# Optimization experiments

Measured on AMD Instinct MI355X. Metric: run time of the kernel, lower is better.

## Reference

```python
import jax, jax.numpy as jnp
import numpy as np

B, T, C_EMB, C_HEAD = 4, 4096, 1024, 64

def setup_inputs() -> dict:
    key = jax.random.key(0)
    kx, kk, kq, kv = jax.random.split(key, 4)
    x = jax.random.normal(kx, (B, T, C_EMB), dtype=jnp.float32)
    # nn.Linear(C_EMB, C_HEAD, bias=False); store as (in, out) so projection is x @ W
    Wk = jax.random.normal(kk, (C_EMB, C_HEAD), dtype=jnp.float32) * 0.02
    Wq = jax.random.normal(kq, (C_EMB, C_HEAD), dtype=jnp.float32) * 0.02
    Wv = jax.random.normal(kv, (C_EMB, C_HEAD), dtype=jnp.float32) * 0.02
    return {"x": x, "Wk": Wk, "Wq": Wq, "Wv": Wv}

def reference(x, Wk, Wq, Wv):
    k = x @ Wk  # [B,T,Ch]
    q = x @ Wq
    v = x @ Wv
    scale = C_HEAD ** -0.5
    weights = jnp.einsum('bqc,bkc->bqk', q, k) * scale  # [B,T,T]
    causal = jnp.tril(jnp.ones((T, T), dtype=bool))
    weights = jnp.where(causal, weights, -jnp.inf)
    # NOTE: original uses F.softmax(dim=1), i.e. over the QUERY (row) axis -> axis=-2
    weights = jax.nn.softmax(weights, axis=-2)
    # dropout_rate=0.0 (eval) -> identity
    return jnp.einsum('bqk,bkc->bqc', weights, v)
```

## Files before the change

### kernel.cpp

```cpp
#include <hip/hip_runtime.h>
#include <math.h>

#define BB 4
#define TT 4096
#define CE 1024
#define CH 64
#define SCALE2 0.18033688011112042f
#define NQT 64
#define NZC 8
#define NZP 4

typedef unsigned short ushort_t;
typedef __attribute__((ext_vector_type(8))) short bf16x8;
typedef __attribute__((ext_vector_type(8))) unsigned short u16x8;
typedef __attribute__((ext_vector_type(4))) float f32x4;

__device__ __forceinline__ unsigned short f2bf(float f) {
    unsigned int x = __builtin_bit_cast(unsigned int, f);
    unsigned int r = x + 0x7fffu + ((x >> 16) & 1u);
    return (unsigned short)(r >> 16);
}
__device__ __forceinline__ float bf2f(unsigned short u) {
    unsigned int x = ((unsigned int)u) << 16;
    return __builtin_bit_cast(float, x);
}

__device__ __forceinline__ void stage_tile(const ushort_t* __restrict__ src,
                                           ushort_t (*dst)[68], int tg)
{
#pragma unroll
    for (int i = 0; i < 2; ++i) {
        const int idx = i * 256 + tg;
        const int row = idx >> 3, c0 = (idx & 7) * 8;
        u16x8 v = *(const u16x8*)(src + (long)idx * 8);
        union { u16x8 v; uint2 q[2]; } uu; uu.v = v;
        *(uint2*)&dst[row][c0]     = uu.q[0];
        *(uint2*)&dst[row][c0 + 4] = uu.q[1];
    }
}

__device__ __forceinline__ void stage_tile512(const ushort_t* __restrict__ src,
                                              ushort_t (*dst)[68], int tid)
{
    const int row = tid >> 3, c0 = (tid & 7) * 8;
    u16x8 v = *(const u16x8*)(src + (long)tid * 8);
    union { u16x8 v; uint2 q[2]; } uu; uu.v = v;
    *(uint2*)&dst[row][c0]     = uu.q[0];
    *(uint2*)&dst[row][c0 + 4] = uu.q[1];
}

__device__ __forceinline__ bf16x8 frag68(const ushort_t* p) {
    union { bf16x8 v; uint2 q[2]; } uu;
    uu.q[0] = *(const uint2*)p;
    uu.q[1] = *(const uint2*)(p + 4);
    return uu.v;
}

__global__ __launch_bounds__(256)
void wt_build(const float* __restrict__ Wk, const float* __restrict__ Wq,
              const float* __restrict__ Wv, ushort_t* __restrict__ wt2)
{
    const int m = blockIdx.x, kt = blockIdx.y;
    const float* __restrict__ W = (m == 0) ? Wk : (m == 1 ? Wq : Wv);
    const int k0 = kt * 64;
    __shared__ float lds[64][65];
    const int cc = threadIdx.x & 63, g = threadIdx.x >> 6;
#pragma unroll
    for (int i = 0; i < 16; ++i) {
        const int r = g * 16 + i;
        lds[r][cc] = W[(k0 + r) * CH + cc];
    }
    __syncthreads();
    const int k = k0 + cc;
#pragma unroll
    for (int i = 0; i < 16; ++i) {
        const int c = g * 16 + i;
        wt2[((long)(k >> 5) * 192 + (m * 64 + c)) * 32 + (k & 31)] = f2bf(lds[cc][c]);
    }
}

__global__ __launch_bounds__(512)
void proj_mfma(const float* __restrict__ x, const ushort_t* __restrict__ wt2,
               ushort_t* __restrict__ qb, ushort_t* __restrict__ kb, ushort_t* __restrict__ vb)
{
    const int tid = threadIdx.x;
    const int w = tid >> 6, l = tid & 63, lg = l >> 4, lr = l & 15;
    const int wr = w >> 2, wc = w & 3;
    const long t0 = (long)blockIdx.x * 32;

    __shared__ ushort_t As[32][68];
    __shared__ ushort_t Bs[192][68];

    f32x4 acc[3];
#pragma unroll
    for (int nf = 0; nf < 3; ++nf) acc[nf] = (f32x4){0.f, 0.f, 0.f, 0.f};

    const int arow = tid >> 4, acol = (tid & 15) * 4;
    const float* __restrict__ xsrc = x + (t0 + arow) * CE + acol;

    int bc[3], bh[3], bk[3];
#pragma unroll
    for (int i = 0; i < 3; ++i) {
        const int idx = i * 512 + tid;
        const int h = idx >= 768;
        const int j = idx - h * 768;
        bc[i] = j >> 2; bh[i] = h; bk[i] = (j & 3) * 8;
    }

    float4 a4 = *(const float4*)(xsrc);
    u16x8 bv[3];
#pragma unroll
    for (int i = 0; i < 3; ++i)
        bv[i] = *(const u16x8*)(wt2 + ((long)(bh[i]) * 192 + bc[i]) * 32 + bk[i]);

    for (int step = 0; step < 16; ++step) {
        {
            uint2 pk;
            pk.x = (unsigned)f2bf(a4.x) | ((unsigned)f2bf(a4.y) << 16);
            pk.y = (unsigned)f2bf(a4.z) | ((unsigned)f2bf(a4.w) << 16);
            *(uint2*)&As[arow][acol] = pk;
#pragma unroll
            for (int i = 0; i < 3; ++i) {
                union { u16x8 v; uint2 q[2]; } uu; uu.v = bv[i];
                ushort_t* d = &Bs[bc[i]][bh[i] * 32 + bk[i]];
                *(uint2*)d = uu.q[0];
                *(uint2*)(d + 4) = uu.q[1];
            }
        }
        __syncthreads();
        if (step < 15) {
            const int k0n = (step + 1) * 64;
            a4 = *(const float4*)(xsrc + k0n);
            const int ktn = k0n >> 5;
#pragma unroll
            for (int i = 0; i < 3; ++i)
                bv[i] = *(const u16x8*)(wt2 + ((long)(ktn + bh[i]) * 192 + bc[i]) * 32 + bk[i]);
        }
#pragma unroll
        for (int h = 0; h < 2; ++h) {
            bf16x8 af = frag68(&As[wr * 16 + lr][h * 32 + lg * 8]);
#pragma unroll
            for (int nf = 0; nf < 3; ++nf) {
                bf16x8 bf = frag68(&Bs[wc * 48 + nf * 16 + lr][h * 32 + lg * 8]);
                acc[nf] = __builtin_amdgcn_mfma_f32_16x16x32_bf16(af, bf, acc[nf], 0, 0, 0);
            }
        }
        __syncthreads();
    }

    ushort_t* Os = &Bs[0][0];
#pragma unroll
    for (int nf = 0; nf < 3; ++nf)
#pragma unroll
        for (int r = 0; r < 4; ++r)
            Os[(wr * 16 + lg * 4 + r) * 200 + wc * 48 + nf * 16 + lr] = f2bf(acc[nf][r]);
    __syncthreads();
    if (tid < 256) {
        const int row = tid >> 3, c0 = (tid & 7) * 8;
#pragma unroll
        for (int m = 0; m < 3; ++m) {
            u16x8 ov = *(const u16x8*)&Os[row * 200 + m * 64 + c0];
            ushort_t* __restrict__ outp = (m == 0) ? kb : (m == 1 ? qb : vb);
            *(u16x8*)(outp + (t0 + row) * CH + c0) = ov;
        }
    }
}

__global__ __launch_bounds__(512)
void colstats_mfma(const ushort_t* __restrict__ qb, const ushort_t* __restrict__ kb,
                   float* __restrict__ pl)
{
    const int b = blockIdx.x, p = blockIdx.y, z = blockIdx.z;
    const int tid = threadIdx.x;
    const int w = tid >> 6, l = tid & 63, lg = l >> 4, lr = l & 15;
    const int wg = w >> 2, wc = w & 3, tg = tid & 255;
    const long baseT = (long)b * TT;
    const long NTT = (long)BB * TT;

    __shared__ ushort_t Ks[64][68], Qs[2][64][68];
    __shared__ float redc[4][64][5];

    for (int pass = 0; pass < 2; ++pass) {
        const int kt = pass ? (63 - p) : p;
        stage_tile512(kb + (baseT + (long)kt * 64) * CH, Ks, tid);
        __syncthreads();
        bf16x8 ka0 = frag68(&Ks[wc * 16 + lr][lg * 8]);
        bf16x8 ka1 = frag68(&Ks[wc * 16 + lr][32 + lg * 8]);

        float l_r[4] = {0.f, 0.f, 0.f, 0.f};

        const int j0 = kt + ((z - kt) & (NZC - 1));
        const int n0 = (j0 < NQT) ? ((NQT - 1 - j0) >> 4) + 1 : 0;
        for (int i = 0; i < n0; ++i) {
            const int j = j0 + NZC * wg + 2 * NZC * i;
            const bool act = (j < NQT);
            if (act) stage_tile(qb + (baseT + (long)j * 64) * CH, Qs[wg], tg);
            __syncthreads();
            if (act) {
                const bool diag = (j == kt);
#pragma unroll
                for (int qf = 0; qf < 4; ++qf) {
                    bf16x8 b0 = frag68(&Qs[wg][qf * 16 + lr][lg * 8]);
                    bf16x8 b1 = frag68(&Qs[wg][qf * 16 + lr][32 + lg * 8]);
                    f32x4 s = {0.f, 0.f, 0.f, 0.f};
                    s = __builtin_amdgcn_mfma_f32_16x16x32_bf16(ka0, b0, s, 0, 0, 0);
                    s = __builtin_amdgcn_mfma_f32_16x16x32_bf16(ka1, b1, s, 0, 0, 0);
#pragma unroll
                    for (int r = 0; r < 4; ++r) {
                        float ev = exp2f(s[r] * SCALE2);
                        if (diag && (qf * 16 + lr) < (wc * 16 + lg * 4 + r)) ev = 0.f;
                        l_r[r] += ev;
                    }
                }
            }
            __syncthreads();
        }
        if (wg == 1) {
#pragma unroll
            for (int r = 0; r < 4; ++r) redc[wc][l][r] = l_r[r];
        }
        __syncthreads();
        if (wg == 0) {
#pragma unroll
            for (int r = 0; r < 4; ++r) {
                float lv = l_r[r] + redc[wc][l][r];
                for (int d = 1; d < 16; d <<= 1) lv += __shfl_xor(lv, d);
                if (lr == 0) {
                    const long k = (long)kt * 64 + wc * 16 + lg * 4 + r;
                    pl[(long)z * NTT + baseT + k] = lv;
                }
            }
        }
        __syncthreads();
    }
}

__global__ __launch_bounds__(256)
void vt_scale(const ushort_t* __restrict__ vb, const float* __restrict__ pl,
              ushort_t* __restrict__ vtb2)
{
    const int b = blockIdx.x;
    const int jt = blockIdx.y;
    const long t0 = (long)jt * 64;
    const int tid = threadIdx.x;
    __shared__ ushort_t lds[64][72];
    const long baseT = (long)b * TT;
    const long NTT = (long)BB * TT;
#pragma unroll
    for (int i = 0; i < 2; ++i) {
        const int t = i * 32 + (tid >> 3);
        const int c0 = (tid & 7) * 8;
        u16x8 v = *(const u16x8*)(vb + (baseT + t0 + t) * CH + c0);
        const long idx = baseT + t0 + t;
        float ls = pl[idx];
#pragma unroll
        for (int zz = 1; zz < NZC; ++zz) ls += pl[zz * NTT + idx];
        const float sc = 1.f / ls;
#pragma unroll
        for (int j = 0; j < 8; ++j) lds[c0 + j][t] = f2bf(bf2f(v[j]) * sc);
    }
    __syncthreads();
    ushort_t* __restrict__ dst = vtb2 + ((long)(b * 64 + jt)) * (64 * 64);
#pragma unroll
    for (int i = 0; i < 2; ++i) {
        const int c = i * 32 + (tid >> 3);
        const int tt0 = (tid & 7) * 8;
        u16x8 ov = *(const u16x8*)&lds[c][tt0];
        *(u16x8*)(dst + (long)c * 64 + tt0) = ov;
    }
}

__global__ __launch_bounds__(512)
void pv_mfma(const ushort_t* __restrict__ qb, const ushort_t* __restrict__ kb,
             const ushort_t* __restrict__ vtb2, float* __restrict__ pout)
{
    const int b = blockIdx.x, p = blockIdx.y, z = blockIdx.z;
    const int tid = threadIdx.x;
    const int w = tid >> 6, l = tid & 63, lg = l >> 4, lr = l & 15;
    const int wg = w >> 2, wc = w & 3, tg = tid & 255;
    const long baseT = (long)b * TT;
    const long NTT = (long)BB * TT;

    __shared__ ushort_t Qs[64][68], Ks[2][64][68], Vs[2][64][68], Ps[2][64][68];
    __shared__ float redp[4][64][17];

    for (int pass = 0; pass < 2; ++pass) {
        const int qt = pass ? (63 - p) : p;
        stage_tile512(qb + (baseT + (long)qt * 64) * CH, Qs, tid);
        __syncthreads();
        bf16x8 qf_[4][2];
#pragma unroll
        for (int qf = 0; qf < 4; ++qf) {
            qf_[qf][0] = frag68(&Qs[qf * 16 + lr][lg * 8]);
            qf_[qf][1] = frag68(&Qs[qf * 16 + lr][32 + lg * 8]);
        }
        f32x4 o[4];
#pragma unroll
        for (int qf = 0; qf < 4; ++qf) o[qf] = (f32x4){0.f, 0.f, 0.f, 0.f};

        const int n0 = (qt >= z) ? ((qt - z) >> 3) + 1 : 0;
        for (int i = 0; i < n0; ++i) {
            const int j = z + 4 * wg + 8 * i;
            const bool act = (j <= qt);
            if (act) {
                stage_tile(kb + (baseT + (long)j * 64) * CH, Ks[wg], tg);
                stage_tile(vtb2 + ((long)(b * 64 + j)) * (64 * 64), Vs[wg], tg);
            }
            __syncthreads();
            bf16x8 va0, va1;
            if (act) {
                bf16x8 ka0 = frag68(&Ks[wg][wc * 16 + lr][lg * 8]);
                bf16x8 ka1 = frag68(&Ks[wg][wc * 16 + lr][32 + lg * 8]);
                va0 = frag68(&Vs[wg][wc * 16 + lr][lg * 8]);
                va1 = frag68(&Vs[wg][wc * 16 + lr][32 + lg * 8]);
                const bool diag = (j == qt);
#pragma unroll
                for (int qf = 0; qf < 4; ++qf) {
                    f32x4 s = {0.f, 0.f, 0.f, 0.f};
                    s = __builtin_amdgcn_mfma_f32_16x16x32_bf16(ka0, qf_[qf][0], s, 0, 0, 0);
                    s = __builtin_amdgcn_mfma_f32_16x16x32_bf16(ka1, qf_[qf][1], s, 0, 0, 0);
                    unsigned short e[4];
#pragma unroll
                    for (int r = 0; r < 4; ++r) {
                        float ev = exp2f(s[r] * SCALE2);
                        if (diag && (qf * 16 + lr) < (wc * 16 + lg * 4 + r)) ev = 0.f;
                        e[r] = f2bf(ev);
                    }
                    uint2 pk;
                    pk.x = (unsigned)e[0] | ((unsigned)e[1] << 16);
                    pk.y = (unsigned)e[2] | ((unsigned)e[3] << 16);
                    *(uint2*)&Ps[wg][qf * 16 + lr][wc * 16 + lg * 4] = pk;
                }
            }
            __syncthreads();
            if (act) {
#pragma unroll
                for (int qf = 0; qf < 4; ++qf) {
                    bf16x8 p0 = frag68(&Ps[wg][qf * 16 + lr][lg * 8]);
                    bf16x8 p1 = frag68(&Ps[wg][qf * 16 + lr][32 + lg * 8]);
                    o[qf] = __builtin_amdgcn_mfma_f32_16x16x32_bf16(va0, p0, o[qf], 0, 0, 0);
                    o[qf] = __builtin_amdgcn_mfma_f32_16x16x32_bf16(va1, p1, o[qf], 0, 0, 0);
                }
            }
        }
        if (wg == 1) {
#pragma unroll
            for (int qf = 0; qf < 4; ++qf)
#pragma unroll
                for (int r = 0; r < 4; ++r) redp[wc][l][qf * 4 + r] = o[qf][r];
        }
        __syncthreads();
        if (wg == 0) {
            float* pz = pout + ((long)z * NTT + baseT + (long)qt * 64) * CH;
#pragma unroll
            for (int qf = 0; qf < 4; ++qf) {
                f32x4 ov = o[qf];
#pragma unroll
                for (int r = 0; r < 4; ++r) ov[r] += redp[wc][l][qf * 4 + r];
                *(f32x4*)(pz + (long)(qf * 16 + lr) * CH + wc * 16 + lg * 4) = ov;
            }
        }
        __syncthreads();
    }
}

__global__ __launch_bounds__(256)
void finalize_out(const float* __restrict__ pout, float* __restrict__ out)
{
    const long i = (long)blockIdx.x * 256 + threadIdx.x;
    const long n4 = (long)BB * TT * CH / 4;
    float4 r = reinterpret_cast<const float4*>(pout)[i];
#pragma unroll
    for (int zz = 1; zz < NZP; ++zz) {
        float4 a = reinterpret_cast<const float4*>(pout)[zz * n4 + i];
        r.x += a.x; r.y += a.y; r.z += a.z; r.w += a.w;
    }
    reinterpret_cast<float4*>(out)[i] = r;
}

extern "C" void kernel_launch(void* const* d_in, const int* in_sizes, int n_in,
                              void* d_out, int out_size, void* d_ws, size_t ws_size,
                              hipStream_t stream)
{
    const float* x  = (const float*)d_in[0];
    const float* Wk = (const float*)d_in[1];
    const float* Wq = (const float*)d_in[2];
    const float* Wv = (const float*)d_in[3];
    float* out = (float*)d_out;

    const size_t NT = (size_t)BB * TT;
    ushort_t* qb   = (ushort_t*)d_ws;
    ushort_t* kb   = qb + NT * CH;
    ushort_t* vb   = kb + NT * CH;
    ushort_t* vtb2 = vb + NT * CH;
    ushort_t* wt2  = vtb2 + NT * CH;
    float* pl   = (float*)(wt2 + 192 * CE);
    float* pout = pl + NZC * NT;

    hipLaunchKernelGGL(wt_build, dim3(3, 16), dim3(256), 0, stream,
                       Wk, Wq, Wv, wt2);
    hipLaunchKernelGGL(proj_mfma, dim3(NT / 32), dim3(512), 0, stream,
                       x, wt2, qb, kb, vb);
    hipLaunchKernelGGL(colstats_mfma, dim3(BB, NQT / 2, NZC), dim3(512), 0, stream,
                       qb, kb, pl);
    hipLaunchKernelGGL(vt_scale, dim3(BB, TT / 64), dim3(256), 0, stream,
                       vb, pl, vtb2);
    hipLaunchKernelGGL(pv_mfma, dim3(BB, NQT / 2, NZP), dim3(512), 0, stream,
                       qb, kb, vtb2, pout);
    hipLaunchKernelGGL(finalize_out, dim3(NT * CH / 4 / 256), dim3(256), 0, stream,
                       pout, out);
}
```

Baseline: 74.42 us.

## Double-buffer LDS in projection and store split-K partials as bf16

The projection kernel now double-buffers its A/B LDS tiles, keeping register prefetch two steps ahead, so each step needs one barrier instead of two. Separately, the pv_mfma split-K partial outputs are stored as bf16 instead of fp32, and finalize_out reads bf16 partials and sums them in fp32. This halves partial-output traffic but adds bf16 rounding to each partial before reduction, which may cost accuracy. The projection also uses twice the LDS per block, which can lower occupancy.

```diff
diff --git a/kernel.cpp b/kernel.cpp
--- a/kernel.cpp
+++ b/kernel.cpp
@@ -88,8 +88,8 @@
     const int wr = w >> 2, wc = w & 3;
     const long t0 = (long)blockIdx.x * 32;
 
-    __shared__ ushort_t As[32][68];
-    __shared__ ushort_t Bs[192][68];
+    __shared__ ushort_t As[2][32][68];
+    __shared__ ushort_t Bs[2][192][68];
 
     f32x4 acc[3];
 #pragma unroll
@@ -112,43 +112,60 @@
 #pragma unroll
     for (int i = 0; i < 3; ++i)
         bv[i] = *(const u16x8*)(wt2 + ((long)(bh[i]) * 192 + bc[i]) * 32 + bk[i]);
+    {
+        uint2 pk;
+        pk.x = (unsigned)f2bf(a4.x) | ((unsigned)f2bf(a4.y) << 16);
+        pk.y = (unsigned)f2bf(a4.z) | ((unsigned)f2bf(a4.w) << 16);
+        *(uint2*)&As[0][arow][acol] = pk;
+#pragma unroll
+        for (int i = 0; i < 3; ++i) {
+            union { u16x8 v; uint2 q[2]; } uu; uu.v = bv[i];
+            ushort_t* d = &Bs[0][bc[i]][bh[i] * 32 + bk[i]];
+            *(uint2*)d = uu.q[0];
+            *(uint2*)(d + 4) = uu.q[1];
+        }
+    }
+    a4 = *(const float4*)(xsrc + 64);
+#pragma unroll
+    for (int i = 0; i < 3; ++i)
+        bv[i] = *(const u16x8*)(wt2 + ((long)(2 + bh[i]) * 192 + bc[i]) * 32 + bk[i]);
+    __syncthreads();
 
     for (int step = 0; step < 16; ++step) {
-        {
+        const int cur = step & 1;
+        if (step + 1 < 16) {
             uint2 pk;
             pk.x = (unsigned)f2bf(a4.x) | ((unsigned)f2bf(a4.y) << 16);
             pk.y = (unsigned)f2bf(a4.z) | ((unsigned)f2bf(a4.w) << 16);
-            *(uint2*)&As[arow][acol] = pk;
+            *(uint2*)&As[cur ^ 1][arow][acol] = pk;
 #pragma unroll
             for (int i = 0; i < 3; ++i) {
                 union { u16x8 v; uint2 q[2]; } uu; uu.v = bv[i];
-                ushort_t* d = &Bs[bc[i]][bh[i] * 32 + bk[i]];
+                ushort_t* d = &Bs[cur ^ 1][bc[i]][bh[i] * 32 + bk[i]];
                 *(uint2*)d = uu.q[0];
                 *(uint2*)(d + 4) = uu.q[1];
             }
         }
-        __syncthreads();
-        if (step < 15) {
-            const int k0n = (step + 1) * 64;
-            a4 = *(const float4*)(xsrc + k0n);
-            const int ktn = k0n >> 5;
+        if (step + 2 < 16) {
+            a4 = *(const float4*)(xsrc + (step + 2) * 64);
+            const int ktn = (step + 2) * 2;
 #pragma unroll
             for (int i = 0; i < 3; ++i)
                 bv[i] = *(const u16x8*)(wt2 + ((long)(ktn + bh[i]) * 192 + bc[i]) * 32 + bk[i]);
         }
 #pragma unroll
         for (int h = 0; h < 2; ++h) {
-            bf16x8 af = frag68(&As[wr * 16 + lr][h * 32 + lg * 8]);
+            bf16x8 af = frag68(&As[cur][wr * 16 + lr][h * 32 + lg * 8]);
 #pragma unroll
             for (int nf = 0; nf < 3; ++nf) {
-                bf16x8 bf = frag68(&Bs[wc * 48 + nf * 16 + lr][h * 32 + lg * 8]);
+                bf16x8 bf = frag68(&Bs[cur][wc * 48 + nf * 16 + lr][h * 32 + lg * 8]);
                 acc[nf] = __builtin_amdgcn_mfma_f32_16x16x32_bf16(af, bf, acc[nf], 0, 0, 0);
             }
         }
         __syncthreads();
     }
 
-    ushort_t* Os = &Bs[0][0];
+    ushort_t* Os = &Bs[0][0][0];
 #pragma unroll
     for (int nf = 0; nf < 3; ++nf)
 #pragma unroll
@@ -272,7 +289,7 @@
 
 __global__ __launch_bounds__(512)
 void pv_mfma(const ushort_t* __restrict__ qb, const ushort_t* __restrict__ kb,
-             const ushort_t* __restrict__ vtb2, float* __restrict__ pout)
+             const ushort_t* __restrict__ vtb2, ushort_t* __restrict__ pout)
 {
     const int b = blockIdx.x, p = blockIdx.y, z = blockIdx.z;
     const int tid = threadIdx.x;
@@ -351,13 +368,16 @@
         }
         __syncthreads();
         if (wg == 0) {
-            float* pz = pout + ((long)z * NTT + baseT + (long)qt * 64) * CH;
+            ushort_t* pz = pout + ((long)z * NTT + baseT + (long)qt * 64) * CH;
 #pragma unroll
             for (int qf = 0; qf < 4; ++qf) {
                 f32x4 ov = o[qf];
 #pragma unroll
                 for (int r = 0; r < 4; ++r) ov[r] += redp[wc][l][qf * 4 + r];
-                *(f32x4*)(pz + (long)(qf * 16 + lr) * CH + wc * 16 + lg * 4) = ov;
+                uint2 pk;
+                pk.x = (unsigned)f2bf(ov[0]) | ((unsigned)f2bf(ov[1]) << 16);
+                pk.y = (unsigned)f2bf(ov[2]) | ((unsigned)f2bf(ov[3]) << 16);
+                *(uint2*)(pz + (long)(qf * 16 + lr) * CH + wc * 16 + lg * 4) = pk;
             }
         }
         __syncthreads();
@@ -365,16 +385,20 @@
 }
 
 __global__ __launch_bounds__(256)
-void finalize_out(const float* __restrict__ pout, float* __restrict__ out)
+void finalize_out(const ushort_t* __restrict__ pout, float* __restrict__ out)
 {
     const long i = (long)blockIdx.x * 256 + threadIdx.x;
-    const long n4 = (long)BB * TT * CH / 4;
-    float4 r = reinterpret_cast<const float4*>(pout)[i];
-#pragma unroll
-    for (int zz = 1; zz < NZP; ++zz) {
-        float4 a = reinterpret_cast<const float4*>(pout)[zz * n4 + i];
-        r.x += a.x; r.y += a.y; r.z += a.z; r.w += a.w;
-    }
+    const long ne = (long)BB * TT * CH;
+    float s0 = 0.f, s1 = 0.f, s2 = 0.f, s3 = 0.f;
+#pragma unroll
+    for (int zz = 0; zz < NZP; ++zz) {
+        uint2 a = *(const uint2*)(pout + zz * ne + i * 4);
+        s0 += bf2f((unsigned short)(a.x & 0xffffu));
+        s1 += bf2f((unsigned short)(a.x >> 16));
+        s2 += bf2f((unsigned short)(a.y & 0xffffu));
+        s3 += bf2f((unsigned short)(a.y >> 16));
+    }
+    float4 r; r.x = s0; r.y = s1; r.z = s2; r.w = s3;
     reinterpret_cast<float4*>(out)[i] = r;
 }
 
@@ -394,8 +418,8 @@
     ushort_t* vb   = kb + NT * CH;
     ushort_t* vtb2 = vb + NT * CH;
     ushort_t* wt2  = vtb2 + NT * CH;
-    float* pl   = (float*)(wt2 + 192 * CE);
-    float* pout = pl + NZC * NT;
+    float* pl      = (float*)(wt2 + 192 * CE);
+    ushort_t* pout = (ushort_t*)(pl + NZC * NT);
 
     hipLaunchKernelGGL(wt_build, dim3(3, 16), dim3(256), 0, stream,
                        Wk, Wq, Wv, wt2);
```

After: 73.44 us. About the same (-1.3%).
